# Kernel tuning notes

Hardware: AMD Instinct MI355X
Metric: run time of the kernel (lower is better)

Reference implementation:

```python
import jax, jax.numpy as jnp
import numpy as np

N, C, D = 64, 4, 2048
K = 64          # kernel_size (shapelet length)
O = 256         # out_channels (number of shapelets)
L = D - K + 1   # number of sliding windows


def setup_inputs() -> dict:
    key = jax.random.key(0)
    k1, k2 = jax.random.split(key)
    x_input = jax.random.normal(k1, (N, C, D), dtype=jnp.float32)
    weight = jax.random.normal(k2, (O, C, K), dtype=jnp.float32)
    return {"x_input": x_input, "weight": weight}


def reference(x_input, weight):
    # im2col: sliding windows of length K -> (n, c, L, K)
    idx = jnp.arange(L)[:, None] + jnp.arange(K)[None, :]  # (L, K)
    windows = x_input[:, :, idx]                            # (n, c, L, K)
    # pairwise squared distances per channel, normalized by K
    x_norm = jnp.sum(windows * windows, axis=-1)            # (n, c, L)
    y_norm = jnp.sum(weight * weight, axis=-1)              # (o, c)
    cross = jnp.einsum('nclk,ock->ncol', windows, weight)   # (n, c, o, L)
    dist = (x_norm[:, :, None, :] + y_norm.T[None, :, :, None] - 2.0 * cross)
    dist = jnp.maximum(dist, 0.0) / K                       # clamp(., 0, inf) / len
    return dist  # (n, in_channels, out_channels, L)
```

## Files before the change

### kernel.cpp

```cpp
#include <hip/hip_runtime.h>

#define N_ 64
#define C_ 4
#define D_ 2048
#define K_ 64
#define O_ 256
#define L_ 1985
#define XSW 2056
#define SPITCH 2008
#define NTILE 125

typedef __attribute__((ext_vector_type(8))) short s16x8;
typedef __attribute__((ext_vector_type(4))) float f32x4;

#define BAR_LGKM() do { \
    asm volatile("s_waitcnt lgkmcnt(0)\n\ts_barrier" ::: "memory"); \
    __builtin_amdgcn_sched_barrier(0); \
} while (0)

__device__ __forceinline__ unsigned short f2bf(float f) {
    union { float f; unsigned u; } v; v.f = f;
    unsigned u = v.u;
    u += 0x7fffu + ((u >> 16) & 1u);
    return (unsigned short)(u >> 16);
}
__device__ __forceinline__ float bflo(unsigned u) {
    union { unsigned x; float f; } v; v.x = u << 16; return v.f;
}
__device__ __forceinline__ float bfhi(unsigned u) {
    union { unsigned x; float f; } v; v.x = u & 0xffff0000u; return v.f;
}

__global__ __launch_bounds__(256) void prep_w(const float* __restrict__ w,
                                              unsigned short* __restrict__ wb,
                                              float* __restrict__ ynK) {
    int o = blockIdx.x;
    int tid = threadIdx.x;
    int c = tid >> 6, k = tid & 63;
    size_t idx = (size_t)(o * C_ + c) * K_ + k;
    float v = w[idx];
    wb[idx] = f2bf(v);
    float s = v * v;
    for (int off = 32; off > 0; off >>= 1) s += __shfl_down(s, off, 64);
    if (k == 0) ynK[o * C_ + c] = s * 0.015625f;
}

__global__ __launch_bounds__(1024) void shapelet_main(const float* __restrict__ x,
                                                      const unsigned short* __restrict__ wb,
                                                      const float* __restrict__ ynK,
                                                      float* __restrict__ out) {
    __shared__ __align__(16) unsigned short xs8[8][XSW];
    __shared__ __align__(16) unsigned short stg[2][16 * SPITCH];

    int nc = blockIdx.x;
    int c = nc & (C_ - 1);
    const float* xrow = x + (size_t)nc * D_;
    int tid = threadIdx.x;

    float* xf   = (float*)stg;
    float* z    = (float*)stg + 2112;
    float* pre  = (float*)stg + 4288;
    float* S16v = (float*)stg + 6400;
    float* xnl  = (float*)stg + 6592;

    for (int i = tid; i < 2112; i += 1024) {
        float v = (i < D_) ? xrow[i] : 0.f;
        xf[i] = v;
        z[i] = v * v;
    }
    __syncthreads();
    for (int j = tid; j < XSW; j += 1024) {
        #pragma unroll
        for (int s = 0; s < 8; ++s) xs8[s][j] = f2bf(xf[j + s]);
    }
    if (tid < 132) {
        float run = 0.f;
        int base = tid * 16;
        #pragma unroll
        for (int j = 0; j < 16; ++j) { pre[base + j] = run; run += z[base + j]; }
        S16v[tid] = run;
    }
    __syncthreads();
    for (int l = tid; l < 2000; l += 1024) {
        int a = l >> 4, b = l & 15;
        float s = S16v[a] - pre[a * 16 + b] + S16v[a + 1] + S16v[a + 2]
                + S16v[a + 3] + pre[(a + 4) * 16 + b];
        xnl[l] = s * 0.015625f;
    }
    __syncthreads();

    int wave = tid >> 6, lane = tid & 63, lr = lane & 15, hi = lane >> 4;
    const unsigned short* xsc = xs8[lr & 7];
    int dj = lane;

    f32x4 xnr[8];
    #pragma unroll
    for (int i = 0; i < 8; ++i) {
        int t = wave + i * 16;
        int tc = t > 124 ? 124 : t;
        xnr[i] = *reinterpret_cast<const f32x4*>(&xnl[tc * 16 + hi * 4]);
    }
    __syncthreads();

    auto drain_band = [&](int b, int pb) {
        float* gb = out + ((size_t)nc * O_ + b * 16 + wave) * L_;
        const unsigned short* src = &stg[pb][wave * SPITCH];
        #pragma unroll
        for (int q = 0; q < 4; ++q) {
            int pos = dj * 8 + q * 512;
            if (pos + 8 <= L_) {
                s16x8 dv = *reinterpret_cast<const s16x8*>(src + pos);
                const unsigned* du = (const unsigned*)&dv;
                f32x4 v0, v1;
                v0[0] = bflo(du[0]); v0[1] = bfhi(du[0]);
                v0[2] = bflo(du[1]); v0[3] = bfhi(du[1]);
                v1[0] = bflo(du[2]); v1[1] = bfhi(du[2]);
                v1[2] = bflo(du[3]); v1[3] = bfhi(du[3]);
                __builtin_memcpy(gb + pos, &v0, 16);
                __builtin_memcpy(gb + pos + 4, &v1, 16);
            }
        }
        if (dj == 0) {
            union { unsigned x; float f; } v; v.x = (unsigned)src[L_ - 1] << 16;
            gb[L_ - 1] = v.f;
        }
    };

    for (int st = 0; st < 16; ++st) {
        int p = st & 1;
        int o = st * 16 + lr;
        const s16x8* wp = reinterpret_cast<const s16x8*>(
            wb + ((size_t)o * C_ + c) * K_ + hi * 8);
        s16x8 w0 = wp[0];
        s16x8 w1 = wp[4];
        float ynKv = ynK[o * C_ + c];

        #pragma unroll
        for (int i = 0; i < 8; ++i) {
            int t = wave + i * 16;
            int tc = t > 124 ? 124 : t;
            int l0t = tc * 16;
            int ja = l0t + (lr & ~7) + hi * 8;
            s16x8 a0 = *reinterpret_cast<const s16x8*>(&xsc[ja]);
            s16x8 a1 = *reinterpret_cast<const s16x8*>(&xsc[ja + 32]);
            f32x4 acc = {0.f, 0.f, 0.f, 0.f};
            acc = __builtin_amdgcn_mfma_f32_16x16x32_bf16(a0, w0, acc, 0, 0, 0);
            acc = __builtin_amdgcn_mfma_f32_16x16x32_bf16(a1, w1, acc, 0, 0, 0);
            f32x4 xv = xnr[i];
            float r0 = fmaxf(fmaf(acc[0], -0.03125f, xv[0] + ynKv), 0.f);
            float r1 = fmaxf(fmaf(acc[1], -0.03125f, xv[1] + ynKv), 0.f);
            float r2 = fmaxf(fmaf(acc[2], -0.03125f, xv[2] + ynKv), 0.f);
            float r3 = fmaxf(fmaf(acc[3], -0.03125f, xv[3] + ynKv), 0.f);
            unsigned long long pk =
                  (unsigned long long)f2bf(r0)
                | ((unsigned long long)f2bf(r1) << 16)
                | ((unsigned long long)f2bf(r2) << 32)
                | ((unsigned long long)f2bf(r3) << 48);
            if (t < NTILE)
                *(unsigned long long*)&stg[p][lr * SPITCH + l0t + hi * 4] = pk;
        }

        if (st > 0) drain_band(st - 1, p ^ 1);
        BAR_LGKM();
    }
    drain_band(15, 1);
}

extern "C" void kernel_launch(void* const* d_in, const int* in_sizes, int n_in,
                              void* d_out, int out_size, void* d_ws, size_t ws_size,
                              hipStream_t stream) {
    const float* x = (const float*)d_in[0];
    const float* w = (const float*)d_in[1];
    float* out = (float*)d_out;

    unsigned short* wb = (unsigned short*)d_ws;
    float* ynK = (float*)((char*)d_ws + (size_t)O_ * C_ * K_ * 2);

    prep_w<<<O_, 256, 0, stream>>>(w, wb, ynK);
    shapelet_main<<<N_ * C_, 1024, 0, stream>>>(x, wb, ynK, out);
}
```

Baseline: 116.0 us.

## Specialize waves into MFMA compute and global-store writer roles

Splits the 16 waves per block into 12 compute waves that run the MFMA distance tiles and 4 writer waves that drain the previous band from LDS to global memory, so compute and stores overlap across waves instead of every wave doing both in turn. The shifted bf16 copies of x shrink from 8 to 4, which means A-operand loads become two 8-byte reads, and xnl moves into its own LDS array read per tile rather than held in registers. In exchange only 12 waves feed the matrix units and each writer wave must store four rows per band, so the writers could become the bottleneck.

```diff
diff --git a/kernel.cpp b/kernel.cpp
--- a/kernel.cpp
+++ b/kernel.cpp
@@ -6,9 +6,11 @@
 #define K_ 64
 #define O_ 256
 #define L_ 1985
-#define XSW 2056
+#define XSW4 2064
 #define SPITCH 2008
 #define NTILE 125
+#define CW 12
+#define NIT 11
 
 typedef __attribute__((ext_vector_type(8))) short s16x8;
 typedef __attribute__((ext_vector_type(4))) float f32x4;
@@ -49,7 +51,8 @@
                                                       const unsigned short* __restrict__ wb,
                                                       const float* __restrict__ ynK,
                                                       float* __restrict__ out) {
-    __shared__ __align__(16) unsigned short xs8[8][XSW];
+    __shared__ __align__(16) unsigned short xs4[4][XSW4];
+    __shared__ float xnl[2000];
     __shared__ __align__(16) unsigned short stg[2][16 * SPITCH];
 
     int nc = blockIdx.x;
@@ -61,7 +64,6 @@
     float* z    = (float*)stg + 2112;
     float* pre  = (float*)stg + 4288;
     float* S16v = (float*)stg + 6400;
-    float* xnl  = (float*)stg + 6592;
 
     for (int i = tid; i < 2112; i += 1024) {
         float v = (i < D_) ? xrow[i] : 0.f;
@@ -69,9 +71,9 @@
         z[i] = v * v;
     }
     __syncthreads();
-    for (int j = tid; j < XSW; j += 1024) {
+    for (int j = tid; j < XSW4; j += 1024) {
         #pragma unroll
-        for (int s = 0; s < 8; ++s) xs8[s][j] = f2bf(xf[j + s]);
+        for (int s = 0; s < 4; ++s) xs4[s][j] = f2bf(xf[j + s]);
     }
     if (tid < 132) {
         float run = 0.f;
@@ -90,63 +92,31 @@
     __syncthreads();
 
     int wave = tid >> 6, lane = tid & 63, lr = lane & 15, hi = lane >> 4;
-    const unsigned short* xsc = xs8[lr & 7];
-    int dj = lane;
+    const unsigned short* xbase = &xs4[lr & 3][(lr & ~3) + hi * 8];
+    bool is_writer = (wave >= CW);
+    int wv = wave - CW;
 
-    f32x4 xnr[8];
-    #pragma unroll
-    for (int i = 0; i < 8; ++i) {
-        int t = wave + i * 16;
-        int tc = t > 124 ? 124 : t;
-        xnr[i] = *reinterpret_cast<const f32x4*>(&xnl[tc * 16 + hi * 4]);
-    }
-    __syncthreads();
-
-    auto drain_band = [&](int b, int pb) {
-        float* gb = out + ((size_t)nc * O_ + b * 16 + wave) * L_;
-        const unsigned short* src = &stg[pb][wave * SPITCH];
-        #pragma unroll
-        for (int q = 0; q < 4; ++q) {
-            int pos = dj * 8 + q * 512;
-            if (pos + 8 <= L_) {
-                s16x8 dv = *reinterpret_cast<const s16x8*>(src + pos);
-                const unsigned* du = (const unsigned*)&dv;
-                f32x4 v0, v1;
-                v0[0] = bflo(du[0]); v0[1] = bfhi(du[0]);
-                v0[2] = bflo(du[1]); v0[3] = bfhi(du[1]);
-                v1[0] = bflo(du[2]); v1[1] = bfhi(du[2]);
-                v1[2] = bflo(du[3]); v1[3] = bfhi(du[3]);
-                __builtin_memcpy(gb + pos, &v0, 16);
-                __builtin_memcpy(gb + pos + 4, &v1, 16);
-            }
-        }
-        if (dj == 0) {
-            union { unsigned x; float f; } v; v.x = (unsigned)src[L_ - 1] << 16;
-            gb[L_ - 1] = v.f;
-        }
-    };
-
-    for (int st = 0; st < 16; ++st) {
-        int p = st & 1;
+    auto compute_band = [&](int st, int p) {
         int o = st * 16 + lr;
         const s16x8* wp = reinterpret_cast<const s16x8*>(
             wb + ((size_t)o * C_ + c) * K_ + hi * 8);
         s16x8 w0 = wp[0];
         s16x8 w1 = wp[4];
         float ynKv = ynK[o * C_ + c];
-
         #pragma unroll
-        for (int i = 0; i < 8; ++i) {
-            int t = wave + i * 16;
+        for (int i = 0; i < NIT; ++i) {
+            int t = wave + i * CW;
             int tc = t > 124 ? 124 : t;
             int l0t = tc * 16;
-            int ja = l0t + (lr & ~7) + hi * 8;
-            s16x8 a0 = *reinterpret_cast<const s16x8*>(&xsc[ja]);
-            s16x8 a1 = *reinterpret_cast<const s16x8*>(&xsc[ja + 32]);
+            union { unsigned long long u[2]; s16x8 v; } a0, a1;
+            const unsigned long long* p0 = (const unsigned long long*)(xbase + l0t);
+            a0.u[0] = p0[0]; a0.u[1] = p0[1];
+            const unsigned long long* p1 = (const unsigned long long*)(xbase + l0t + 32);
+            a1.u[0] = p1[0]; a1.u[1] = p1[1];
             f32x4 acc = {0.f, 0.f, 0.f, 0.f};
-            acc = __builtin_amdgcn_mfma_f32_16x16x32_bf16(a0, w0, acc, 0, 0, 0);
-            acc = __builtin_amdgcn_mfma_f32_16x16x32_bf16(a1, w1, acc, 0, 0, 0);
-            f32x4 xv = xnr[i];
+            acc = __builtin_amdgcn_mfma_f32_16x16x32_bf16(a0.v, w0, acc, 0, 0, 0);
+            acc = __builtin_amdgcn_mfma_f32_16x16x32_bf16(a1.v, w1, acc, 0, 0, 0);
+            f32x4 xv = *reinterpret_cast<const f32x4*>(&xnl[l0t + hi * 4]);
             float r0 = fmaxf(fmaf(acc[0], -0.03125f, xv[0] + ynKv), 0.f);
             float r1 = fmaxf(fmaf(acc[1], -0.03125f, xv[1] + ynKv), 0.f);
             float r2 = fmaxf(fmaf(acc[2], -0.03125f, xv[2] + ynKv), 0.f);
@@ -159,11 +129,43 @@
             if (t < NTILE)
                 *(unsigned long long*)&stg[p][lr * SPITCH + l0t + hi * 4] = pk;
         }
+    };
 
-        if (st > 0) drain_band(st - 1, p ^ 1);
+    auto drain_band = [&](int b, int pb) {
+        #pragma unroll
+        for (int rr = 0; rr < 4; ++rr) {
+            int r = wv * 4 + rr;
+            float* gb = out + ((size_t)nc * O_ + b * 16 + r) * L_;
+            const unsigned short* src = &stg[pb][r * SPITCH];
+            #pragma unroll
+            for (int q = 0; q < 4; ++q) {
+                int pos = lane * 8 + q * 512;
+                if (pos + 8 <= L_) {
+                    s16x8 dv = *reinterpret_cast<const s16x8*>(src + pos);
+                    const unsigned* du = (const unsigned*)&dv;
+                    f32x4 v0, v1;
+                    v0[0] = bflo(du[0]); v0[1] = bfhi(du[0]);
+                    v0[2] = bflo(du[1]); v0[3] = bfhi(du[1]);
+                    v1[0] = bflo(du[2]); v1[1] = bfhi(du[2]);
+                    v1[2] = bflo(du[3]); v1[3] = bfhi(du[3]);
+                    __builtin_memcpy(gb + pos, &v0, 16);
+                    __builtin_memcpy(gb + pos + 4, &v1, 16);
+                }
+            }
+            if (lane == 0) {
+                union { unsigned x; float f; } v; v.x = (unsigned)src[L_ - 1] << 16;
+                gb[L_ - 1] = v.f;
+            }
+        }
+    };
+
+    for (int st = 0; st < 16; ++st) {
+        int p = st & 1;
+        if (!is_writer) compute_band(st, p);
+        else if (st > 0) drain_band(st - 1, p ^ 1);
         BAR_LGKM();
     }
-    drain_band(15, 1);
+    if (is_writer) drain_band(15, 1);
 }
 
 extern "C" void kernel_launch(void* const* d_in, const int* in_sizes, int n_in,
```

Measured after the change: 112.3 us. 1.03x faster.
